# Performance work log

Measured on AMD Instinct MI355X. Metric: run time of the kernel, lower is better.

## Reference

```python
import jax, jax.numpy as jnp
import numpy as np

TAU = 0.05
EPS = 1e-12


def _l2_normalize(x):
    # F.normalize(p=2): x / max(||x||, eps)
    n = jnp.sqrt(jnp.sum(x * x, axis=-1, keepdims=True))
    return x / jnp.maximum(n, EPS)


def _masked_lse(sim, mask):
    # logsumexp over axis -1 restricted to mask; rows with empty mask are
    # masked out downstream (has_pos), so we guard the log to stay finite.
    neg_inf = jnp.finfo(sim.dtype).min
    mx = jnp.max(jnp.where(mask, sim, neg_inf), axis=-1)
    mx_safe = jnp.where(mx > neg_inf / 2, mx, 0.0)
    s = jnp.sum(jnp.where(mask, jnp.exp(sim - mx_safe[:, None]), 0.0), axis=-1)
    return mx_safe + jnp.log(jnp.where(s > 0, s, 1.0))


def setup_inputs() -> dict:
    key = jax.random.key(0)
    k1, k2, k3, k4 = jax.random.split(key, 4)
    B, S, D = 64, 128, 256
    return {
        "logits": jax.random.normal(k1, (B, S, D), dtype=jnp.float32),
        "labels": jax.random.normal(k2, (B, S, D), dtype=jnp.float32),
        "pad_mask": jax.random.randint(k3, (B, S), 0, 2, dtype=jnp.int32),
        "ad_idxs": jax.random.randint(k4, (B, S), 0, 500, dtype=jnp.int32),
    }


def reference(logits, labels, pad_mask, ad_idxs):
    B, S, D = logits.shape
    q = _l2_normalize(logits.reshape(B * S, D))
    k = _l2_normalize(labels.reshape(B * S, D))
    valid = pad_mask.reshape(B * S).astype(bool)
    ad = ad_idxs.reshape(B * S)

    sim = jnp.einsum("nd,md->nm", q, k) / TAU          # [N, N]
    pair_valid = valid[None, :] & valid[:, None]
    pos_mask = (ad[None, :] == ad[:, None]) & pair_valid

    pos_lse = _masked_lse(sim, pos_mask)
    all_lse = _masked_lse(sim, pair_valid)
    has_pos = jnp.any(pos_mask, axis=-1)

    loss_per_row = -(pos_lse - all_lse)
    # mean over rows with at least one positive (== loss_per_row[has_pos].mean())
    cnt = jnp.sum(has_pos.astype(sim.dtype))
    loss = jnp.sum(jnp.where(has_pos, loss_per_row, 0.0)) / jnp.maximum(cnt, 1.0)
    return loss
```

## Files before the change

### kernel.cpp

```cpp
#include <hip/hip_runtime.h>
#include <hip/hip_bf16.h>
#include <hip/hip_fp8.h>
#include <math.h>

typedef float f32x4 __attribute__((ext_vector_type(4)));
typedef int   i32x4 __attribute__((ext_vector_type(4)));
typedef int   v8i   __attribute__((ext_vector_type(8)));

constexpr int Nn = 8192;
constexpr int Dd = 256;
constexpr float LOG2E     = 1.4426950408889634f;
constexpr float SIM_SCALE = 20.0f * LOG2E;
constexpr float SIM_BIAS  = -20.0f * LOG2E;
constexpr int   SCALE1    = 0x7F7F7F7F;

typedef __attribute__((address_space(1))) const unsigned int gu32;
typedef __attribute__((address_space(3))) unsigned int lu32;
__device__ __forceinline__ void gload16(const unsigned char* g, unsigned char* l) {
  __builtin_amdgcn_global_load_lds((gu32*)(uintptr_t)g, (lu32*)(uintptr_t)l, 16, 0, 0);
}

__global__ __launch_bounds__(256) void prep_kernel(const float* __restrict__ logits,
                                                   const float* __restrict__ labels,
                                                   const int* __restrict__ pad,
                                                   unsigned char* __restrict__ qb,
                                                   unsigned char* __restrict__ kb,
                                                   float* __restrict__ cbias,
                                                   float* __restrict__ g_all,
                                                   float* __restrict__ g_pos) {
  const int j = blockIdx.x * 256 + threadIdx.x;
  if (j < Nn) {
    cbias[j] = pad[j] ? 0.0f : -1e30f;
    g_all[j] = 0.0f;
    g_pos[j] = 0.0f;
  }

  const int gw   = (blockIdx.x * 256 + threadIdx.x) >> 6;
  const int lane = threadIdx.x & 63;
  const float* src;
  unsigned char* dst;
  int row;
  if (gw < Nn) { src = logits; dst = qb; row = gw; }
  else         { src = labels; dst = kb; row = gw - Nn; }

  const float4 v = *reinterpret_cast<const float4*>(src + (size_t)row * Dd + lane * 4);
  float ss = v.x * v.x + v.y * v.y + v.z * v.z + v.w * v.w;
#pragma unroll
  for (int m = 32; m >= 1; m >>= 1) ss += __shfl_xor(ss, m);
  const float scale = 1.0f / fmaxf(sqrtf(ss), 1e-12f);

  const __hip_fp8_e4m3 e0(v.x * scale);
  const __hip_fp8_e4m3 e1(v.y * scale);
  const __hip_fp8_e4m3 e2(v.z * scale);
  const __hip_fp8_e4m3 e3(v.w * scale);
  const unsigned int packed = (unsigned int)e0.__x |
                              ((unsigned int)e1.__x << 8) |
                              ((unsigned int)e2.__x << 16) |
                              ((unsigned int)e3.__x << 24);
  reinterpret_cast<unsigned int*>(dst + (size_t)row * Dd)[lane] = packed;
}

__global__ __launch_bounds__(256) void gemm_lse_kernel(const unsigned char* __restrict__ qb,
                                                       const unsigned char* __restrict__ kb,
                                                       const float* __restrict__ cbias,
                                                       const int* __restrict__ ad,
                                                       float* __restrict__ g_all,
                                                       float* __restrict__ g_pos) {
  __shared__ unsigned char smem[32768];
  unsigned char* As = smem;
  unsigned char* Bs = smem + 16384;
  float* redA = reinterpret_cast<float*>(smem);
  float* redP = reinterpret_cast<float*>(smem) + 4096;

  const int tid  = threadIdx.x;
  const int lane = tid & 63;
  const int w    = tid >> 6;
  const int wrow = (w >> 1) * 64;
  const int wcol = (w & 1) * 64;
  const int lq   = lane & 15;
  const int qd   = lane >> 4;
  const int rowBase = blockIdx.x * 128;
  const int colBase = blockIdx.y * 128;

  const int srl = lane >> 3;
  const int cg  = (lane & 7) ^ srl;
  const unsigned char* gA0 = qb + (size_t)(rowBase + w * 32 + srl) * Dd + cg * 16;
  const unsigned char* gB0 = kb + (size_t)(colBase + w * 32 + srl) * Dd + cg * 16;

  f32x4 c[4][4];
#pragma unroll
  for (int mt = 0; mt < 4; ++mt)
#pragma unroll
    for (int nt = 0; nt < 4; ++nt)
      c[mt][nt] = (f32x4){0.f, 0.f, 0.f, 0.f};

  for (int kk = 0; kk < 2; ++kk) {
    const int kOff = kk * 128;
    __syncthreads();
#pragma unroll
    for (int i = 0; i < 4; ++i) {
      gload16(gA0 + (size_t)i * 8 * Dd + kOff, &As[(w * 32 + i * 8) * 128]);
      gload16(gB0 + (size_t)i * 8 * Dd + kOff, &Bs[(w * 32 + i * 8) * 128]);
    }
    __syncthreads();

    const int g0 = qd << 1;
    v8i af[4];
#pragma unroll
    for (int mt = 0; mt < 4; ++mt) {
      const int r = wrow + mt * 16 + lq;
      const i32x4 lo = *reinterpret_cast<const i32x4*>(&As[r * 128 + ((g0 ^ (r & 7)) << 4)]);
      const i32x4 hi = *reinterpret_cast<const i32x4*>(&As[r * 128 + (((g0 + 1) ^ (r & 7)) << 4)]);
      af[mt] = (v8i){lo.x, lo.y, lo.z, lo.w, hi.x, hi.y, hi.z, hi.w};
    }
#pragma unroll
    for (int nt = 0; nt < 4; ++nt) {
      const int r = wcol + nt * 16 + lq;
      const i32x4 lo = *reinterpret_cast<const i32x4*>(&Bs[r * 128 + ((g0 ^ (r & 7)) << 4)]);
      const i32x4 hi = *reinterpret_cast<const i32x4*>(&Bs[r * 128 + (((g0 + 1) ^ (r & 7)) << 4)]);
      const v8i bfq = (v8i){lo.x, lo.y, lo.z, lo.w, hi.x, hi.y, hi.z, hi.w};
#pragma unroll
      for (int mt = 0; mt < 4; ++mt)
        c[mt][nt] = __builtin_amdgcn_mfma_scale_f32_16x16x128_f8f6f4(
            af[mt], bfq, c[mt][nt], 0, 0, 0, SCALE1, 0, SCALE1);
    }
  }

  float colB[4];
  int colAd[4];
#pragma unroll
  for (int nt = 0; nt < 4; ++nt) {
    const int col = colBase + wcol + nt * 16 + lq;
    colB[nt]  = SIM_BIAS + cbias[col];
    colAd[nt] = ad[col];
  }

  __syncthreads();

  const int idx = (w & 1) * 16 + lq;
  const int g   = idx >> 2;
  const int gi  = idx & 3;

#pragma unroll
  for (int mt = 0; mt < 4; ++mt) {
#pragma unroll
    for (int r = 0; r < 4; ++r) {
      const int row   = wrow + mt * 16 + qd * 4 + r;
      const int rowAd = ad[rowBase + row];
      float a = 0.f, p = 0.f;
#pragma unroll
      for (int nt = 0; nt < 4; ++nt) {
        const float e = __builtin_amdgcn_exp2f(fmaf(c[mt][nt][r], SIM_SCALE, colB[nt]));
        a += e;
        p += (colAd[nt] == rowAd) ? e : 0.f;
      }
      const int off = row * 32 + ((g ^ (row & 7)) << 2) + gi;
      redA[off] = a;
      redP[off] = p;
    }
  }
  __syncthreads();

  if (tid < 128) {
    const int row = tid;
    float a = 0.f, p = 0.f;
#pragma unroll
    for (int gg = 0; gg < 8; ++gg) {
      const int off = row * 32 + ((gg ^ (row & 7)) << 2);
      const f32x4 va = *reinterpret_cast<const f32x4*>(&redA[off]);
      const f32x4 vp = *reinterpret_cast<const f32x4*>(&redP[off]);
      a += (va[0] + va[1]) + (va[2] + va[3]);
      p += (vp[0] + vp[1]) + (vp[2] + vp[3]);
    }
    atomicAdd(&g_all[rowBase + row], a);
    atomicAdd(&g_pos[rowBase + row], p);
  }
}

__global__ __launch_bounds__(1024) void reduce_kernel(const float* __restrict__ g_all,
                                                      const float* __restrict__ g_pos,
                                                      const int* __restrict__ pad,
                                                      float* __restrict__ out) {
  __shared__ float sS[16], sC[16];
  const int t = threadIdx.x;
  float s = 0.f, c = 0.f;
  const float4* ga4 = (const float4*)g_all;
  const float4* gp4 = (const float4*)g_pos;
  const int4*   pd4 = (const int4*)pad;
  for (int i = t; i < Nn / 4; i += 1024) {
    const float4 ga = ga4[i];
    const float4 gp = gp4[i];
    const int4   pd = pd4[i];
    if (pd.x) { s += __logf(ga.x) - __logf(gp.x); c += 1.f; }
    if (pd.y) { s += __logf(ga.y) - __logf(gp.y); c += 1.f; }
    if (pd.z) { s += __logf(ga.z) - __logf(gp.z); c += 1.f; }
    if (pd.w) { s += __logf(ga.w) - __logf(gp.w); c += 1.f; }
  }
#pragma unroll
  for (int m = 32; m >= 1; m >>= 1) {
    s += __shfl_xor(s, m);
    c += __shfl_xor(c, m);
  }
  if ((t & 63) == 0) { sS[t >> 6] = s; sC[t >> 6] = c; }
  __syncthreads();
  if (t == 0) {
    float S = 0.f, C = 0.f;
#pragma unroll
    for (int i = 0; i < 16; ++i) { S += sS[i]; C += sC[i]; }
    out[0] = S / fmaxf(C, 1.0f);
  }
}

extern "C" void kernel_launch(void* const* d_in, const int* in_sizes, int n_in,
                              void* d_out, int out_size, void* d_ws, size_t ws_size,
                              hipStream_t stream) {
  const float* logits = (const float*)d_in[0];
  const float* labels = (const float*)d_in[1];
  const int*   pad    = (const int*)d_in[2];
  const int*   ad     = (const int*)d_in[3];

  char* ws = (char*)d_ws;
  unsigned char* qb = (unsigned char*)(ws);
  unsigned char* kb = (unsigned char*)(ws + 2097152);
  float*  cb   = (float*)(ws + 4194304);
  float*  gAll = (float*)(ws + 4227072);
  float*  gPos = (float*)(ws + 4259840);
  float*  out  = (float*)d_out;

  prep_kernel<<<4096, 256, 0, stream>>>(logits, labels, pad, qb, kb, cb, gAll, gPos);
  gemm_lse_kernel<<<dim3(64, 64), 256, 0, stream>>>(qb, kb, cb, ad, gAll, gPos);
  reduce_kernel<<<1, 1024, 0, stream>>>(gAll, gPos, pad, out);
}
```

Baseline: 104.5 us.

## Keep full-K B tile resident in LDS and process two row tiles per block

Each block now loads the complete 128x256 B (key) tile into LDS once and loops over two 128-row A tiles, halving the grid and the redundant B loads. The SIM_BIAS is folded into cbias during prep, and the per-row partial sums are pre-reduced with a lane shuffle so the LDS reduction buffer is halved. LDS per block grows to 48KB, which may reduce occupancy, and the two passes run serially inside a block with extra barriers.

New measurement: 118.4 us. +13.2%, slower.

```diff
diff --git a/kernel.cpp b/kernel.cpp
--- a/kernel.cpp
+++ b/kernel.cpp
@@ -30,7 +30,7 @@
                                                    float* __restrict__ g_pos) {
   const int j = blockIdx.x * 256 + threadIdx.x;
   if (j < Nn) {
-    cbias[j] = pad[j] ? 0.0f : -1e30f;
+    cbias[j] = pad[j] ? SIM_BIAS : -1e30f;
     g_all[j] = 0.0f;
     g_pos[j] = 0.0f;
   }
@@ -66,11 +66,10 @@
                                                        const int* __restrict__ ad,
                                                        float* __restrict__ g_all,
                                                        float* __restrict__ g_pos) {
-  __shared__ unsigned char smem[32768];
+  __shared__ unsigned char smem[49152];
   unsigned char* As = smem;
-  unsigned char* Bs = smem + 16384;
   float* redA = reinterpret_cast<float*>(smem);
-  float* redP = reinterpret_cast<float*>(smem) + 4096;
+  float* redP = reinterpret_cast<float*>(smem) + 2048;
 
   const int tid  = threadIdx.x;
   const int lane = tid & 63;
@@ -79,7 +78,7 @@
   const int wcol = (w & 1) * 64;
   const int lq   = lane & 15;
   const int qd   = lane >> 4;
-  const int rowBase = blockIdx.x * 128;
+  const int rowBase = blockIdx.x * 256;
   const int colBase = blockIdx.y * 128;
 
   const int srl = lane >> 3;
@@ -87,93 +86,107 @@
   const unsigned char* gA0 = qb + (size_t)(rowBase + w * 32 + srl) * Dd + cg * 16;
   const unsigned char* gB0 = kb + (size_t)(colBase + w * 32 + srl) * Dd + cg * 16;
 
-  f32x4 c[4][4];
-#pragma unroll
-  for (int mt = 0; mt < 4; ++mt)
-#pragma unroll
-    for (int nt = 0; nt < 4; ++nt)
-      c[mt][nt] = (f32x4){0.f, 0.f, 0.f, 0.f};
-
-  for (int kk = 0; kk < 2; ++kk) {
-    const int kOff = kk * 128;
+#pragma unroll
+  for (int kkb = 0; kkb < 2; ++kkb)
+#pragma unroll
+    for (int i = 0; i < 4; ++i)
+      gload16(gB0 + (size_t)i * 8 * Dd + kkb * 128,
+              &smem[16384 + kkb * 16384 + (w * 32 + i * 8) * 128]);
+
+  float colB[4];
+  int colAd[4];
+#pragma unroll
+  for (int nt = 0; nt < 4; ++nt) {
+    const int col = colBase + wcol + nt * 16 + lq;
+    colB[nt]  = cbias[col];
+    colAd[nt] = ad[col];
+  }
+
+  for (int pass = 0; pass < 2; ++pass) {
+    const int rowOff = pass * 128;
+
+    f32x4 c[4][4];
+#pragma unroll
+    for (int mt = 0; mt < 4; ++mt)
+#pragma unroll
+      for (int nt = 0; nt < 4; ++nt)
+        c[mt][nt] = (f32x4){0.f, 0.f, 0.f, 0.f};
+
+    for (int kk = 0; kk < 2; ++kk) {
+      const int kOff = kk * 128;
+      __syncthreads();
+#pragma unroll
+      for (int i = 0; i < 4; ++i)
+        gload16(gA0 + (size_t)(rowOff + i * 8) * Dd + kOff,
+                &As[(w * 32 + i * 8) * 128]);
+      __syncthreads();
+
+      const int g0 = qd << 1;
+      v8i af[4];
+#pragma unroll
+      for (int mt = 0; mt < 4; ++mt) {
+        const int r = wrow + mt * 16 + lq;
+        const i32x4 lo = *reinterpret_cast<const i32x4*>(&As[r * 128 + ((g0 ^ (r & 7)) << 4)]);
+        const i32x4 hi = *reinterpret_cast<const i32x4*>(&As[r * 128 + (((g0 + 1) ^ (r & 7)) << 4)]);
+        af[mt] = (v8i){lo.x, lo.y, lo.z, lo.w, hi.x, hi.y, hi.z, hi.w};
+      }
+      const unsigned char* BsH = &smem[16384 + kk * 16384];
+#pragma unroll
+      for (int nt = 0; nt < 4; ++nt) {
+        const int r = wcol + nt * 16 + lq;
+        const i32x4 lo = *reinterpret_cast<const i32x4*>(&BsH[r * 128 + ((g0 ^ (r & 7)) << 4)]);
+        const i32x4 hi = *reinterpret_cast<const i32x4*>(&BsH[r * 128 + (((g0 + 1) ^ (r & 7)) << 4)]);
+        const v8i bfq = (v8i){lo.x, lo.y, lo.z, lo.w, hi.x, hi.y, hi.z, hi.w};
+#pragma unroll
+        for (int mt = 0; mt < 4; ++mt)
+          c[mt][nt] = __builtin_amdgcn_mfma_scale_f32_16x16x128_f8f6f4(
+              af[mt], bfq, c[mt][nt], 0, 0, 0, SCALE1, 0, SCALE1);
+      }
+    }
+
     __syncthreads();
-#pragma unroll
-    for (int i = 0; i < 4; ++i) {
-      gload16(gA0 + (size_t)i * 8 * Dd + kOff, &As[(w * 32 + i * 8) * 128]);
-      gload16(gB0 + (size_t)i * 8 * Dd + kOff, &Bs[(w * 32 + i * 8) * 128]);
+
+#pragma unroll
+    for (int mt = 0; mt < 4; ++mt) {
+#pragma unroll
+      for (int r = 0; r < 4; ++r) {
+        const int row   = wrow + mt * 16 + qd * 4 + r;
+        const int rowAd = ad[rowBase + rowOff + row];
+        float a = 0.f, p = 0.f;
+#pragma unroll
+        for (int nt = 0; nt < 4; ++nt) {
+          const float e = __builtin_amdgcn_exp2f(fmaf(c[mt][nt][r], SIM_SCALE, colB[nt]));
+          a += e;
+          p += (colAd[nt] == rowAd) ? e : 0.f;
+        }
+        a += __shfl_xor(a, 8);
+        p += __shfl_xor(p, 8);
+        if (lq < 8) {
+          const int idx = (w & 1) * 8 + lq;
+          const int g   = idx >> 2;
+          const int gi  = idx & 3;
+          const int off = row * 16 + ((g ^ (row & 3)) << 2) + gi;
+          redA[off] = a;
+          redP[off] = p;
+        }
+      }
     }
     __syncthreads();
 
-    const int g0 = qd << 1;
-    v8i af[4];
-#pragma unroll
-    for (int mt = 0; mt < 4; ++mt) {
-      const int r = wrow + mt * 16 + lq;
-      const i32x4 lo = *reinterpret_cast<const i32x4*>(&As[r * 128 + ((g0 ^ (r & 7)) << 4)]);
-      const i32x4 hi = *reinterpret_cast<const i32x4*>(&As[r * 128 + (((g0 + 1) ^ (r & 7)) << 4)]);
-      af[mt] = (v8i){lo.x, lo.y, lo.z, lo.w, hi.x, hi.y, hi.z, hi.w};
+    if (tid < 128) {
+      const int row = tid;
+      float a = 0.f, p = 0.f;
+#pragma unroll
+      for (int gg = 0; gg < 4; ++gg) {
+        const int off = row * 16 + ((gg ^ (row & 3)) << 2);
+        const f32x4 va = *reinterpret_cast<const f32x4*>(&redA[off]);
+        const f32x4 vp = *reinterpret_cast<const f32x4*>(&redP[off]);
+        a += (va[0] + va[1]) + (va[2] + va[3]);
+        p += (vp[0] + vp[1]) + (vp[2] + vp[3]);
+      }
+      atomicAdd(&g_all[rowBase + rowOff + row], a);
+      atomicAdd(&g_pos[rowBase + rowOff + row], p);
     }
-#pragma unroll
-    for (int nt = 0; nt < 4; ++nt) {
-      const int r = wcol + nt * 16 + lq;
-      const i32x4 lo = *reinterpret_cast<const i32x4*>(&Bs[r * 128 + ((g0 ^ (r & 7)) << 4)]);
-      const i32x4 hi = *reinterpret_cast<const i32x4*>(&Bs[r * 128 + (((g0 + 1) ^ (r & 7)) << 4)]);
-      const v8i bfq = (v8i){lo.x, lo.y, lo.z, lo.w, hi.x, hi.y, hi.z, hi.w};
-#pragma unroll
-      for (int mt = 0; mt < 4; ++mt)
-        c[mt][nt] = __builtin_amdgcn_mfma_scale_f32_16x16x128_f8f6f4(
-            af[mt], bfq, c[mt][nt], 0, 0, 0, SCALE1, 0, SCALE1);
-    }
-  }
-
-  float colB[4];
-  int colAd[4];
-#pragma unroll
-  for (int nt = 0; nt < 4; ++nt) {
-    const int col = colBase + wcol + nt * 16 + lq;
-    colB[nt]  = SIM_BIAS + cbias[col];
-    colAd[nt] = ad[col];
-  }
-
-  __syncthreads();
-
-  const int idx = (w & 1) * 16 + lq;
-  const int g   = idx >> 2;
-  const int gi  = idx & 3;
-
-#pragma unroll
-  for (int mt = 0; mt < 4; ++mt) {
-#pragma unroll
-    for (int r = 0; r < 4; ++r) {
-      const int row   = wrow + mt * 16 + qd * 4 + r;
-      const int rowAd = ad[rowBase + row];
-      float a = 0.f, p = 0.f;
-#pragma unroll
-      for (int nt = 0; nt < 4; ++nt) {
-        const float e = __builtin_amdgcn_exp2f(fmaf(c[mt][nt][r], SIM_SCALE, colB[nt]));
-        a += e;
-        p += (colAd[nt] == rowAd) ? e : 0.f;
-      }
-      const int off = row * 32 + ((g ^ (row & 7)) << 2) + gi;
-      redA[off] = a;
-      redP[off] = p;
-    }
-  }
-  __syncthreads();
-
-  if (tid < 128) {
-    const int row = tid;
-    float a = 0.f, p = 0.f;
-#pragma unroll
-    for (int gg = 0; gg < 8; ++gg) {
-      const int off = row * 32 + ((gg ^ (row & 7)) << 2);
-      const f32x4 va = *reinterpret_cast<const f32x4*>(&redA[off]);
-      const f32x4 vp = *reinterpret_cast<const f32x4*>(&redP[off]);
-      a += (va[0] + va[1]) + (va[2] + va[3]);
-      p += (vp[0] + vp[1]) + (vp[2] + vp[3]);
-    }
-    atomicAdd(&g_all[rowBase + row], a);
-    atomicAdd(&g_pos[rowBase + row], p);
   }
 }
 
@@ -228,6 +241,6 @@
   float*  out  = (float*)d_out;
 
   prep_kernel<<<4096, 256, 0, stream>>>(logits, labels, pad, qb, kb, cb, gAll, gPos);
-  gemm_lse_kernel<<<dim3(64, 64), 256, 0, stream>>>(qb, kb, cb, ad, gAll, gPos);
+  gemm_lse_kernel<<<dim3(32, 64), 256, 0, stream>>>(qb, kb, cb, ad, gAll, gPos);
   reduce_kernel<<<1, 1024, 0, stream>>>(gAll, gPos, pad, out);
 }
```
